# Optimization experiments

Hardware: AMD Instinct MI355X
Metric: run time of the kernel (lower is better)

Reference implementation:

```python
import jax, jax.numpy as jnp
import numpy as np

T = 8192
N = 2048
SPECTRAL_RADIUS = 0.9
WASHOUT = 200


def setup_inputs() -> dict:
    key = jax.random.key(0)
    ku, kin, kres = jax.random.split(key, 3)
    u = jax.random.normal(ku, (T,), dtype=jnp.float32)
    W_in = jax.random.normal(kin, (N,), dtype=jnp.float32)
    W_res = np.asarray(jax.random.normal(kres, (N, N), dtype=jnp.float32))
    # __init__: rescale reservoir to target spectral radius
    spec_rad = float(np.max(np.abs(np.linalg.eigvals(W_res.astype(np.float64)))))
    if spec_rad != 0:
        W_res = W_res * (SPECTRAL_RADIUS / spec_rad)
    return {
        "u": u,
        "W_in": W_in,
        "W_res": jnp.asarray(W_res, dtype=jnp.float32),
        "washout": WASHOUT,
    }


def reference(u, W_in, W_res, washout):
    # Sequential ESN recurrence: x_t = tanh(W_in * u_t + W_res @ x_{t-1})
    n = W_res.shape[0]

    def step(x, u_t):
        x_new = jnp.tanh(W_in * u_t + W_res @ x)  # [N]
        return x_new, x_new

    x0 = jnp.zeros((n,), dtype=W_res.dtype)
    _, X = jax.lax.scan(step, x0, u)  # X: [T, N]
    return X[washout:]  # states after washout (fed to the readout)
```

## Files before the change

kernel.cpp:

```cpp
#include <hip/hip_runtime.h>

#define TSTEPS 8192
#define NDIM   2048
#define NBLK   128
#define NTHR   1024
#define RPB    16
#define NREP   16

typedef float    f32x4 __attribute__((ext_vector_type(4)));
typedef unsigned u32x4 __attribute__((ext_vector_type(4)));

__device__ __forceinline__ unsigned ld_u32_agent(const unsigned* p) {
  return __hip_atomic_load((unsigned*)p, __ATOMIC_RELAXED, __HIP_MEMORY_SCOPE_AGENT);
}
__device__ __forceinline__ void st_u32_agent(unsigned* p, unsigned v) {
  __hip_atomic_store(p, v, __ATOMIC_RELAXED, __HIP_MEMORY_SCOPE_AGENT);
}
__device__ __forceinline__ u32x4 ld_x4_agent(const u32x4* p) {
  u32x4 r;
  asm volatile("global_load_dwordx4 %0, %1, off sc1\n\ts_waitcnt vmcnt(0)"
               : "=v"(r) : "v"(p) : "memory");
  return r;
}
__device__ __forceinline__ void st_x4_agent(u32x4* p, u32x4 v) {
  asm volatile("global_store_dwordx4 %0, %1, off sc1" :: "v"(p), "v"(v) : "memory");
}
__device__ __forceinline__ f32x4 ld_w_sync(const f32x4* p) {
  f32x4 r;
  asm volatile("global_load_dwordx4 %0, %1, off\n\ts_waitcnt vmcnt(0)"
               : "=v"(r) : "v"(p));
  return r;
}

__global__ void __launch_bounds__(NTHR, 1) esn_persistent(
    const float* __restrict__ u,
    const float* __restrict__ W_in,
    const float* __restrict__ W_res,
    const int* __restrict__ washout_p,
    float* __restrict__ out,
    unsigned* __restrict__ ws)
{
  const int tid  = threadIdx.x;
  const int bid  = blockIdx.x;
  const int wave = tid >> 6;
  const int lane = tid & 63;
  const int row  = bid * RPB + wave;
  const int washout = washout_p[0];

  unsigned* abortw  = ws + 144;
  unsigned* repbase = ws + 256;

  __shared__ __align__(16) float    x_lds[NDIM];
  __shared__ __align__(16) unsigned xpack_lds[RPB];
  __shared__ __align__(16) float    xval_lds[RPB];
  __shared__ int s_abort;
  if (tid == 0) s_abort = 0;

  const f32x4* Wr = (const f32x4*)(W_res + (size_t)row * NDIM) + lane;
  const f32x4 w0 = ld_w_sync(Wr + 0 * 64), w1 = ld_w_sync(Wr + 1 * 64);
  const f32x4 w2 = ld_w_sync(Wr + 2 * 64), w3 = ld_w_sync(Wr + 3 * 64);
  const f32x4 w4 = ld_w_sync(Wr + 4 * 64), w5 = ld_w_sync(Wr + 5 * 64);
  const f32x4 w6 = ld_w_sync(Wr + 6 * 64), w7 = ld_w_sync(Wr + 7 * 64);
  const float win = W_in[row];

  unsigned* myrep0 = repbase + ((unsigned)(bid & (NREP - 1)) * 2) * NDIM;

  for (int t = 0; t < TSTEPS; ++t) {
    if (tid < 512) {
      const u32x4* src = (const u32x4*)(myrep0 + (t & 1) * NDIM) + tid;
      const unsigned want = (unsigned)t;
      u32x4 r;
      bool ok;
      {
        unsigned g = 0;
        do {
          r = ld_x4_agent(src);
          ok = ((((r.x ^ want) | (r.y ^ want)) |
                 ((r.z ^ want) | (r.w ^ want))) & 0xFFFFu) == 0u;
          if (!ok && ((++g & 255u) == 0u)) {
            if (ld_u32_agent(abortw) != 0u) break;
            if (g > (1u << 20)) { st_u32_agent(abortw, 1u); break; }
          }
        } while (!ok);
      }
      if (!ok) s_abort = 1;
      f32x4 xv;
      xv.x = __uint_as_float(r.x & 0xFFFF0000u);
      xv.y = __uint_as_float(r.y & 0xFFFF0000u);
      xv.z = __uint_as_float(r.z & 0xFFFF0000u);
      xv.w = __uint_as_float(r.w & 0xFFFF0000u);
      ((f32x4*)x_lds)[tid] = xv;
    }
    const float ut = u[t];
    __syncthreads();
    if (s_abort) return;

    float a0 = 0.f, b0 = 0.f;
    const f32x4* x4v = (const f32x4*)x_lds + lane;
#define ESN_DOT(WA, K, A) { const f32x4 xv = x4v[(K) * 64];                   \
      A += WA.x * xv.x; A += WA.y * xv.y; A += WA.z * xv.z; A += WA.w * xv.w; }
    ESN_DOT(w0, 0, a0) ESN_DOT(w1, 1, b0)
    ESN_DOT(w2, 2, a0) ESN_DOT(w3, 3, b0)
    ESN_DOT(w4, 4, a0) ESN_DOT(w5, 5, b0)
    ESN_DOT(w6, 6, a0) ESN_DOT(w7, 7, b0)
#undef ESN_DOT
    float c = a0 + b0;
#pragma unroll
    for (int off = 32; off > 0; off >>= 1) c += __shfl_xor(c, off, 64);

    if (lane == 0) {
      const float pre = win * ut + c;
      const float e2  = __expf(2.0f * pre);
      const float th  = 1.0f - __fdividef(2.0f, e2 + 1.0f);
      xval_lds[wave] = th;
      const unsigned b  = __float_as_uint(th);
      const unsigned bf = (b + 0x7fffu + ((b >> 16) & 1u)) & 0xFFFF0000u;
      xpack_lds[wave] = bf | (unsigned)(t + 1);
    }
    __syncthreads();

    if (tid < 4 * NREP) {
      const int rep = tid >> 2, seg = tid & 3;
      u32x4* dst = (u32x4*)(repbase + ((unsigned)(rep * 2 + ((t + 1) & 1)) * NDIM))
                   + bid * 4 + seg;
      st_x4_agent(dst, ((const u32x4*)xpack_lds)[seg]);
    } else if (tid >= 64 && tid < 68 && t >= washout) {
      float4* orow = (float4*)(out + (size_t)(t - washout) * NDIM) + bid * 4 + (tid - 64);
      const f32x4 vv = ((const f32x4*)xval_lds)[tid - 64];
      float4 v; v.x = vv.x; v.y = vv.y; v.z = vv.z; v.w = vv.w;
      *orow = v;
    }
  }
}

extern "C" void kernel_launch(void* const* d_in, const int* in_sizes, int n_in,
                              void* d_out, int out_size, void* d_ws, size_t ws_size,
                              hipStream_t stream) {
  const float* u       = (const float*)d_in[0];
  const float* W_in    = (const float*)d_in[1];
  const float* W_res   = (const float*)d_in[2];
  const int*   washout = (const int*)d_in[3];
  float*       out     = (float*)d_out;

  (void)hipMemsetAsync(d_ws, 0, 1024 + NREP * 2 * NDIM * 4, stream);

  esn_persistent<<<dim3(NBLK), dim3(NTHR), 0, stream>>>(
      u, W_in, W_res, washout, out, (unsigned*)d_ws);
}
```

Measured before the change: 17.13 ms.

## Remove block barriers: each wave polls full state and computes four rows

Cuts the block from 16 waves to 4 and gives each wave four reservoir rows. Every wave now polls the whole replicated bf16-tagged state vector straight into registers with eight batched loads, so the LDS staging and both __syncthreads per timestep go away. Each wave publishes its four packed results to all replicas on its own. The aim is to take intra-block barrier latency off the sequential critical path, at the cost of four times more polling traffic per wave and much higher register use per thread.

```diff
diff --git a/kernel.cpp b/kernel.cpp
--- a/kernel.cpp
+++ b/kernel.cpp
@@ -3,7 +3,7 @@
 #define TSTEPS 8192
 #define NDIM   2048
 #define NBLK   128
-#define NTHR   1024
+#define NTHR   256
 #define RPB    16
 #define NREP   16
 
@@ -16,12 +16,6 @@
 __device__ __forceinline__ void st_u32_agent(unsigned* p, unsigned v) {
   __hip_atomic_store(p, v, __ATOMIC_RELAXED, __HIP_MEMORY_SCOPE_AGENT);
 }
-__device__ __forceinline__ u32x4 ld_x4_agent(const u32x4* p) {
-  u32x4 r;
-  asm volatile("global_load_dwordx4 %0, %1, off sc1\n\ts_waitcnt vmcnt(0)"
-               : "=v"(r) : "v"(p) : "memory");
-  return r;
-}
 __device__ __forceinline__ void st_x4_agent(u32x4* p, u32x4 v) {
   asm volatile("global_store_dwordx4 %0, %1, off sc1" :: "v"(p), "v"(v) : "memory");
 }
@@ -30,6 +24,24 @@
   asm volatile("global_load_dwordx4 %0, %1, off\n\ts_waitcnt vmcnt(0)"
                : "=v"(r) : "v"(p));
   return r;
+}
+__device__ __forceinline__ void ld8(unsigned long long sb, unsigned va, unsigned vb,
+                                    u32x4& r0, u32x4& r1, u32x4& r2, u32x4& r3,
+                                    u32x4& r4, u32x4& r5, u32x4& r6, u32x4& r7) {
+  asm volatile(
+    "global_load_dwordx4 %0, %[va], %[sb] offset:0    sc1\n\t"
+    "global_load_dwordx4 %1, %[va], %[sb] offset:1024 sc1\n\t"
+    "global_load_dwordx4 %2, %[va], %[sb] offset:2048 sc1\n\t"
+    "global_load_dwordx4 %3, %[va], %[sb] offset:3072 sc1\n\t"
+    "global_load_dwordx4 %4, %[vb], %[sb] offset:0    sc1\n\t"
+    "global_load_dwordx4 %5, %[vb], %[sb] offset:1024 sc1\n\t"
+    "global_load_dwordx4 %6, %[vb], %[sb] offset:2048 sc1\n\t"
+    "global_load_dwordx4 %7, %[vb], %[sb] offset:3072 sc1\n\t"
+    "s_waitcnt vmcnt(0)"
+    : "=&v"(r0), "=&v"(r1), "=&v"(r2), "=&v"(r3),
+      "=&v"(r4), "=&v"(r5), "=&v"(r6), "=&v"(r7)
+    : [sb]"s"(sb), [va]"v"(va), [vb]"v"(vb)
+    : "memory");
 }
 
 __global__ void __launch_bounds__(NTHR, 1) esn_persistent(
@@ -44,91 +56,95 @@
   const int bid  = blockIdx.x;
   const int wave = tid >> 6;
   const int lane = tid & 63;
-  const int row  = bid * RPB + wave;
+  const int rowbase = bid * RPB + wave * 4;
   const int washout = washout_p[0];
 
   unsigned* abortw  = ws + 144;
   unsigned* repbase = ws + 256;
 
-  __shared__ __align__(16) float    x_lds[NDIM];
-  __shared__ __align__(16) unsigned xpack_lds[RPB];
-  __shared__ __align__(16) float    xval_lds[RPB];
-  __shared__ int s_abort;
-  if (tid == 0) s_abort = 0;
+  const f32x4* Wr0 = (const f32x4*)(W_res + (size_t)(rowbase + 0) * NDIM) + lane;
+  const f32x4* Wr1 = (const f32x4*)(W_res + (size_t)(rowbase + 1) * NDIM) + lane;
+  const f32x4* Wr2 = (const f32x4*)(W_res + (size_t)(rowbase + 2) * NDIM) + lane;
+  const f32x4* Wr3 = (const f32x4*)(W_res + (size_t)(rowbase + 3) * NDIM) + lane;
+  const f32x4 w00 = ld_w_sync(Wr0+0*64), w01 = ld_w_sync(Wr0+1*64), w02 = ld_w_sync(Wr0+2*64), w03 = ld_w_sync(Wr0+3*64);
+  const f32x4 w04 = ld_w_sync(Wr0+4*64), w05 = ld_w_sync(Wr0+5*64), w06 = ld_w_sync(Wr0+6*64), w07 = ld_w_sync(Wr0+7*64);
+  const f32x4 w10 = ld_w_sync(Wr1+0*64), w11 = ld_w_sync(Wr1+1*64), w12 = ld_w_sync(Wr1+2*64), w13 = ld_w_sync(Wr1+3*64);
+  const f32x4 w14 = ld_w_sync(Wr1+4*64), w15 = ld_w_sync(Wr1+5*64), w16 = ld_w_sync(Wr1+6*64), w17 = ld_w_sync(Wr1+7*64);
+  const f32x4 w20 = ld_w_sync(Wr2+0*64), w21 = ld_w_sync(Wr2+1*64), w22 = ld_w_sync(Wr2+2*64), w23 = ld_w_sync(Wr2+3*64);
+  const f32x4 w24 = ld_w_sync(Wr2+4*64), w25 = ld_w_sync(Wr2+5*64), w26 = ld_w_sync(Wr2+6*64), w27 = ld_w_sync(Wr2+7*64);
+  const f32x4 w30 = ld_w_sync(Wr3+0*64), w31 = ld_w_sync(Wr3+1*64), w32 = ld_w_sync(Wr3+2*64), w33 = ld_w_sync(Wr3+3*64);
+  const f32x4 w34 = ld_w_sync(Wr3+4*64), w35 = ld_w_sync(Wr3+5*64), w36 = ld_w_sync(Wr3+6*64), w37 = ld_w_sync(Wr3+7*64);
+  const float win0 = W_in[rowbase + 0], win1 = W_in[rowbase + 1];
+  const float win2 = W_in[rowbase + 2], win3 = W_in[rowbase + 3];
 
-  const f32x4* Wr = (const f32x4*)(W_res + (size_t)row * NDIM) + lane;
-  const f32x4 w0 = ld_w_sync(Wr + 0 * 64), w1 = ld_w_sync(Wr + 1 * 64);
-  const f32x4 w2 = ld_w_sync(Wr + 2 * 64), w3 = ld_w_sync(Wr + 3 * 64);
-  const f32x4 w4 = ld_w_sync(Wr + 4 * 64), w5 = ld_w_sync(Wr + 5 * 64);
-  const f32x4 w6 = ld_w_sync(Wr + 6 * 64), w7 = ld_w_sync(Wr + 7 * 64);
-  const float win = W_in[row];
+  const unsigned myrep = (unsigned)(bid & (NREP - 1)) * 2u * NDIM;
+  const unsigned va = (unsigned)lane * 16u;
+  const unsigned vb = va + 4096u;
 
-  unsigned* myrep0 = repbase + ((unsigned)(bid & (NREP - 1)) * 2) * NDIM;
+  unsigned g = 0;
+  for (int t = 0; t < TSTEPS; ++t) {
+    const float ut = u[t];
+    const unsigned long long sb =
+        (unsigned long long)(size_t)(repbase + myrep + (unsigned)(t & 1) * NDIM);
+    const unsigned want = (unsigned)t & 0xFFFFu;
+    u32x4 r0, r1, r2, r3, r4, r5, r6, r7;
+    bool dead = false;
+    for (;;) {
+      ld8(sb, va, vb, r0, r1, r2, r3, r4, r5, r6, r7);
+#define CHK(R) ((R.x ^ want) | (R.y ^ want) | (R.z ^ want) | (R.w ^ want))
+      const unsigned d = CHK(r0) | CHK(r1) | CHK(r2) | CHK(r3)
+                       | CHK(r4) | CHK(r5) | CHK(r6) | CHK(r7);
+#undef CHK
+      if (__all((d & 0xFFFFu) == 0u)) break;
+      if ((++g & 255u) == 0u) {
+        if (ld_u32_agent(abortw) != 0u) { dead = true; break; }
+        if (g > (1u << 20)) { st_u32_agent(abortw, 1u); dead = true; break; }
+      }
+    }
+    if (dead) return;
 
-  for (int t = 0; t < TSTEPS; ++t) {
-    if (tid < 512) {
-      const u32x4* src = (const u32x4*)(myrep0 + (t & 1) * NDIM) + tid;
-      const unsigned want = (unsigned)t;
-      u32x4 r;
-      bool ok;
-      {
-        unsigned g = 0;
-        do {
-          r = ld_x4_agent(src);
-          ok = ((((r.x ^ want) | (r.y ^ want)) |
-                 ((r.z ^ want) | (r.w ^ want))) & 0xFFFFu) == 0u;
-          if (!ok && ((++g & 255u) == 0u)) {
-            if (ld_u32_agent(abortw) != 0u) break;
-            if (g > (1u << 20)) { st_u32_agent(abortw, 1u); break; }
-          }
-        } while (!ok);
-      }
-      if (!ok) s_abort = 1;
-      f32x4 xv;
-      xv.x = __uint_as_float(r.x & 0xFFFF0000u);
-      xv.y = __uint_as_float(r.y & 0xFFFF0000u);
-      xv.z = __uint_as_float(r.z & 0xFFFF0000u);
-      xv.w = __uint_as_float(r.w & 0xFFFF0000u);
-      ((f32x4*)x_lds)[tid] = xv;
+#define UNP(R) { __uint_as_float(R.x & 0xFFFF0000u), __uint_as_float(R.y & 0xFFFF0000u), \
+                 __uint_as_float(R.z & 0xFFFF0000u), __uint_as_float(R.w & 0xFFFF0000u) }
+    const f32x4 x0 = UNP(r0), x1 = UNP(r1), x2 = UNP(r2), x3 = UNP(r3);
+    const f32x4 x4 = UNP(r4), x5 = UNP(r5), x6 = UNP(r6), x7 = UNP(r7);
+#undef UNP
+
+    float a0 = 0.f, a1 = 0.f, a2 = 0.f, a3 = 0.f;
+#define DOTC(W, X, A) { A += W.x*X.x; A += W.y*X.y; A += W.z*X.z; A += W.w*X.w; }
+    DOTC(w00,x0,a0) DOTC(w01,x1,a0) DOTC(w02,x2,a0) DOTC(w03,x3,a0)
+    DOTC(w04,x4,a0) DOTC(w05,x5,a0) DOTC(w06,x6,a0) DOTC(w07,x7,a0)
+    DOTC(w10,x0,a1) DOTC(w11,x1,a1) DOTC(w12,x2,a1) DOTC(w13,x3,a1)
+    DOTC(w14,x4,a1) DOTC(w15,x5,a1) DOTC(w16,x6,a1) DOTC(w17,x7,a1)
+    DOTC(w20,x0,a2) DOTC(w21,x1,a2) DOTC(w22,x2,a2) DOTC(w23,x3,a2)
+    DOTC(w24,x4,a2) DOTC(w25,x5,a2) DOTC(w26,x6,a2) DOTC(w27,x7,a2)
+    DOTC(w30,x0,a3) DOTC(w31,x1,a3) DOTC(w32,x2,a3) DOTC(w33,x3,a3)
+    DOTC(w34,x4,a3) DOTC(w35,x5,a3) DOTC(w36,x6,a3) DOTC(w37,x7,a3)
+#undef DOTC
+#pragma unroll
+    for (int off = 32; off > 0; off >>= 1) {
+      a0 += __shfl_xor(a0, off, 64);
+      a1 += __shfl_xor(a1, off, 64);
+      a2 += __shfl_xor(a2, off, 64);
+      a3 += __shfl_xor(a3, off, 64);
     }
-    const float ut = u[t];
-    __syncthreads();
-    if (s_abort) return;
 
-    float a0 = 0.f, b0 = 0.f;
-    const f32x4* x4v = (const f32x4*)x_lds + lane;
-#define ESN_DOT(WA, K, A) { const f32x4 xv = x4v[(K) * 64];                   \
-      A += WA.x * xv.x; A += WA.y * xv.y; A += WA.z * xv.z; A += WA.w * xv.w; }
-    ESN_DOT(w0, 0, a0) ESN_DOT(w1, 1, b0)
-    ESN_DOT(w2, 2, a0) ESN_DOT(w3, 3, b0)
-    ESN_DOT(w4, 4, a0) ESN_DOT(w5, 5, b0)
-    ESN_DOT(w6, 6, a0) ESN_DOT(w7, 7, b0)
-#undef ESN_DOT
-    float c = a0 + b0;
-#pragma unroll
-    for (int off = 32; off > 0; off >>= 1) c += __shfl_xor(c, off, 64);
+#define FIN(WI, A) (1.0f - __fdividef(2.0f, __expf(2.0f * ((WI) * ut + (A))) + 1.0f))
+    const float t0 = FIN(win0, a0), t1 = FIN(win1, a1);
+    const float t2 = FIN(win2, a2), t3 = FIN(win3, a3);
+#undef FIN
+    const unsigned tag = (unsigned)(t + 1);
+#define PCK(V) (((__float_as_uint(V) + 0x7fffu + ((__float_as_uint(V) >> 16) & 1u)) \
+                 & 0xFFFF0000u) | tag)
+    u32x4 P; P.x = PCK(t0); P.y = PCK(t1); P.z = PCK(t2); P.w = PCK(t3);
+#undef PCK
 
-    if (lane == 0) {
-      const float pre = win * ut + c;
-      const float e2  = __expf(2.0f * pre);
-      const float th  = 1.0f - __fdividef(2.0f, e2 + 1.0f);
-      xval_lds[wave] = th;
-      const unsigned b  = __float_as_uint(th);
-      const unsigned bf = (b + 0x7fffu + ((b >> 16) & 1u)) & 0xFFFF0000u;
-      xpack_lds[wave] = bf | (unsigned)(t + 1);
-    }
-    __syncthreads();
-
-    if (tid < 4 * NREP) {
-      const int rep = tid >> 2, seg = tid & 3;
-      u32x4* dst = (u32x4*)(repbase + ((unsigned)(rep * 2 + ((t + 1) & 1)) * NDIM))
-                   + bid * 4 + seg;
-      st_x4_agent(dst, ((const u32x4*)xpack_lds)[seg]);
-    } else if (tid >= 64 && tid < 68 && t >= washout) {
-      float4* orow = (float4*)(out + (size_t)(t - washout) * NDIM) + bid * 4 + (tid - 64);
-      const f32x4 vv = ((const f32x4*)xval_lds)[tid - 64];
-      float4 v; v.x = vv.x; v.y = vv.y; v.z = vv.z; v.w = vv.w;
-      *orow = v;
+    if (lane < NREP) {
+      u32x4* dst = (u32x4*)(repbase + ((unsigned)lane * 2u + (unsigned)((t + 1) & 1)) * NDIM)
+                   + (bid * 4 + wave);
+      st_x4_agent(dst, P);
+    } else if (lane == 16 && t >= washout) {
+      float4 ov; ov.x = t0; ov.y = t1; ov.z = t2; ov.w = t3;
+      *(float4*)(out + (size_t)(t - washout) * NDIM + rowbase) = ov;
     }
   }
 }
```

Result: slower. 35.62 ms (+108.0%).
